# Optimization experiments

Hardware: AMD Instinct MI355X
Metric: run time of the kernel (lower is better)

Reference implementation:

```python
import jax, jax.numpy as jnp
import numpy as np
from jax import lax

NUM_CLASSES = 21
MAX_OUT = 5          # max_output_size in tf.image.non_max_suppression
IOU_THR = 0.5        # NMS_IOU_THRESHOLD
CONF_THR = 0.5       # CONFIDENCE_THRESHOLD
NEG = -1e9           # stand-in for -inf score (suppressed / background)


def setup_inputs() -> dict:
    key = jax.random.key(0)
    k1, k2, k3 = jax.random.split(key, 3)
    B, N, C = 128, 8732, NUM_CLASSES
    logits = jax.random.normal(k1, (B, N, 4 + C), dtype=jnp.float32)
    # default boxes in corner format [ymin, xmin, ymax, xmax], valid geometry
    ctr = jax.random.uniform(k2, (N, 2), dtype=jnp.float32)                 # cy, cx
    sz = jax.random.uniform(k3, (N, 2), dtype=jnp.float32, minval=0.05, maxval=0.3)  # h, w
    default_boxes = jnp.clip(
        jnp.concatenate([ctr - sz / 2, ctr + sz / 2], axis=-1), 0.0, 1.0)
    return {"logits": logits, "default_boxes": default_boxes}


def _decode(loc, db):
    # db: [N,4] corners -> center/size (matches get_offset's tf.stack)
    cy = (db[:, 2] + db[:, 0]) / 2
    cx = (db[:, 3] + db[:, 1]) / 2
    h = db[:, 2] - db[:, 0]
    w = db[:, 3] - db[:, 1]
    # loc: [B,N,4] = (dy, dx, dh, dw)
    ncy = loc[..., 0] * h + cy
    ncx = loc[..., 1] * w + cx
    nh = jnp.exp(loc[..., 2]) * h
    nw = jnp.exp(loc[..., 3]) * w
    boxes = jnp.stack(
        [ncy - nh / 2, ncx - nw / 2, ncy + nh / 2, ncx + nw / 2], axis=-1)
    return jnp.clip(boxes, 0.0, 1.0)


def _iou_one_vs_all(box, boxes):
    # box [4], boxes [N,4], corner format
    tl = jnp.maximum(box[:2], boxes[:, :2])
    br = jnp.minimum(box[2:], boxes[:, 2:])
    wh = jnp.maximum(br - tl, 0.0)
    inter = wh[:, 0] * wh[:, 1]
    a1 = (box[2] - box[0]) * (box[3] - box[1])
    a2 = (boxes[:, 2] - boxes[:, 0]) * (boxes[:, 3] - boxes[:, 1])
    return inter / (a1 + a2 - inter + 1e-12)


def _nms_single(boxes, scores, classes_f):
    # boxes [N,4], scores [N] (background already set to NEG), classes_f [N] float
    def step(s, _):
        i = jnp.argmax(s)
        sc = s[i]
        b = boxes[i]
        valid = sc > CONF_THR  # score_threshold in tf NMS
        iou = _iou_one_vs_all(b, boxes)
        s = jnp.where(iou > IOU_THR, NEG, s)  # suppresses i too (IoU=1)
        return s, (b, classes_f[i], sc, valid)

    _, (bs, cs, ss, vs) = lax.scan(step, scores, None, length=MAX_OUT)
    # pad invalid slots with zeros (TF returns variable-length; we use fixed 5 + zero pad)
    bs = jnp.where(vs[:, None], bs, 0.0)
    cs = jnp.where(vs, cs, 0.0)
    ss = jnp.where(vs, ss, 0.0)
    return bs, cs[:, None], ss[:, None]  # [5,4], [5,1], [5,1]


def reference(logits, default_boxes):
    boxes = _decode(logits[..., :4], default_boxes)          # [B,N,4]
    probs = jax.nn.softmax(logits[..., 4:], axis=-1)         # [B,N,C]
    scores = jnp.max(probs, axis=-1)                          # [B,N]
    classes = jnp.argmax(probs, axis=-1)                      # [B,N] int
    # boolean_mask(classes != 0) expressed as score = -inf for background
    scores_eff = jnp.where(classes != 0, scores, NEG)
    det_b, det_c, det_s = jax.vmap(_nms_single)(
        boxes, scores_eff, classes.astype(jnp.float32))
    # pack detection_boxes / detection_classes / detection_scores -> [B,5,6]
    return jnp.concatenate([det_b, det_c, det_s], axis=-1)
```

## Files before the change

### kernel.cpp

```cpp
#include <hip/hip_runtime.h>

#define NEG (-1e9f)
constexpr int NCLS   = 21;
constexpr int NBOX   = 8732;
constexpr int MAXOUT = 5;
constexpr int CAP    = NBOX;
constexpr float IOU_THR  = 0.5f;
constexpr float CONF_THR = 0.5f;

__global__ __launch_bounds__(256) void decode_kernel(
        const float* __restrict__ logits,
        const float4* __restrict__ dbox4,
        float4* __restrict__ cand,
        int* __restrict__ cnt,
        int BN) {
    __shared__ float sl[4][64 * 25];
    const int t    = threadIdx.x;
    const int wave = t >> 6;
    const int lane = t & 63;
    float* slw = sl[wave];

    const long long waveBox = ((long long)blockIdx.x * 4 + wave) * 64;
    if (waveBox >= BN) return;
    const long long gF     = waveBox * 25;
    const long long totalF = (long long)BN * 25;

    if (waveBox + 64 <= BN) {
        const float* gbase = logits + gF;
#pragma unroll
        for (int c = 0; c < 25; c++) {
            __builtin_amdgcn_global_load_lds(
                (const __attribute__((address_space(1))) void*)(gbase + c * 64 + lane),
                (__attribute__((address_space(3))) void*)(slw + c * 64),
                4, 0, 0);
        }
    } else {
        for (int j = lane; j < 64 * 25; j += 64) {
            long long g = gF + j;
            slw[j] = (g < totalF) ? logits[g] : 0.f;
        }
    }
    __builtin_amdgcn_s_waitcnt(0x0F70);
    __builtin_amdgcn_sched_barrier(0);

    const long long i = waveBox + lane;
    if (i >= BN) return;
    const float* L = slw + lane * 25;
    const int n = (int)(i % NBOX);
    const int b = (int)(i / NBOX);

    float4 db = dbox4[n];
    float cy = (db.z + db.x) * 0.5f;
    float cx = (db.w + db.y) * 0.5f;
    float h  = db.z - db.x;
    float w  = db.w - db.y;
    float ncy = L[0] * h + cy;
    float ncx = L[1] * w + cx;
    float nh  = expf(L[2]) * h;
    float nw  = expf(L[3]) * w;
    float y1 = fminf(fmaxf(ncy - nh * 0.5f, 0.f), 1.f);
    float x1 = fminf(fmaxf(ncx - nw * 0.5f, 0.f), 1.f);
    float y2 = fminf(fmaxf(ncy + nh * 0.5f, 0.f), 1.f);
    float x2 = fminf(fmaxf(ncx + nw * 0.5f, 0.f), 1.f);

    float m = L[4];
    int am = 0;
#pragma unroll
    for (int j = 1; j < NCLS; j++) {
        float x = L[4 + j];
        if (x > m) { m = x; am = j; }
    }
    float sum = 0.f;
#pragma unroll
    for (int j = 0; j < NCLS; j++) sum += expf(L[4 + j] - m);
    float score = 1.0f / sum;

    if (am != 0 && score > CONF_THR) {
        int p = atomicAdd(&cnt[b], 1);
        if (p < CAP) {
            float4* c = cand + ((long long)b * CAP + p) * 2;
            c[0] = make_float4(y1, x1, y2, x2);
            c[1] = make_float4(score, (float)am, (float)n, 0.f);
        }
    }
}

__global__ __launch_bounds__(64) void nms_kernel(
        const float4* __restrict__ cand,
        const int* __restrict__ cnt,
        float* __restrict__ out) {
    const int b    = blockIdx.x;
    const int lane = threadIdx.x;
    __shared__ float s_sc[CAP];
    __shared__ float s_id[CAP];

    const int M = min(cnt[b], CAP);
    const float4* cb = cand + (long long)b * CAP * 2;
    float* o = out + (long long)b * MAXOUT * 6;

    for (int i = lane; i < M; i += 64) {
        float4 mrec = cb[i * 2 + 1];
        s_sc[i] = mrec.x;
        s_id[i] = mrec.z;
    }

    int k = 0;
    for (; k < MAXOUT; k++) {
        float bv = -INFINITY, boid = 3.0e38f;
        int bi = -1;
        for (int i = lane; i < M; i += 64) {
            float v = s_sc[i], oid = s_id[i];
            if (v > bv || (v == bv && oid < boid)) { bv = v; boid = oid; bi = i; }
        }
        for (int mm = 32; mm >= 1; mm >>= 1) {
            float v2 = __shfl_xor(bv,   mm, 64);
            float o2 = __shfl_xor(boid, mm, 64);
            int   i2 = __shfl_xor(bi,   mm, 64);
            if (v2 > bv || (v2 == bv && o2 < boid)) { bv = v2; boid = o2; bi = i2; }
        }
        if (bi < 0 || !(bv > CONF_THR)) break;

        float4 sb = cb[bi * 2];
        if (lane == 0) {
            float4 mm2 = cb[bi * 2 + 1];
            o[k * 6 + 0] = sb.x; o[k * 6 + 1] = sb.y;
            o[k * 6 + 2] = sb.z; o[k * 6 + 3] = sb.w;
            o[k * 6 + 4] = mm2.y; o[k * 6 + 5] = bv;
        }

        float a1 = (sb.z - sb.x) * (sb.w - sb.y);
        for (int i = lane; i < M; i += 64) {
            float4 c = cb[i * 2];
            float tly = fmaxf(sb.x, c.x);
            float tlx = fmaxf(sb.y, c.y);
            float bry = fminf(sb.z, c.z);
            float brx = fminf(sb.w, c.w);
            float wh0 = fmaxf(bry - tly, 0.f);
            float wh1 = fmaxf(brx - tlx, 0.f);
            float inter = wh0 * wh1;
            float a2 = (c.z - c.x) * (c.w - c.y);
            float iou = inter / (a1 + a2 - inter + 1e-12f);
            if (iou > IOU_THR) s_sc[i] = NEG;
        }
    }
    for (int j = k * 6 + lane; j < MAXOUT * 6; j += 64) o[j] = 0.f;
}

extern "C" void kernel_launch(void* const* d_in, const int* in_sizes, int n_in,
                              void* d_out, int out_size, void* d_ws, size_t ws_size,
                              hipStream_t stream) {
    const float* logits = (const float*)d_in[0];
    const float4* dbox4 = (const float4*)d_in[1];
    float* out          = (float*)d_out;

    const int N  = in_sizes[1] / 4;
    const int B  = in_sizes[0] / (N * 25);
    const int BN = B * N;

    int* cnt = (int*)d_ws;
    float4* cand = (float4*)((char*)d_ws + (((size_t)B * sizeof(int) + 15) & ~(size_t)15));

    hipMemsetAsync(cnt, 0, (size_t)B * sizeof(int), stream);
    decode_kernel<<<(BN + 255) / 256, 256, 0, stream>>>(logits, dbox4, cand, cnt, BN);
    nms_kernel<<<B, 64, 0, stream>>>(cand, cnt, out);
}
```

Before: 194.8 us.

## Load four boxes per thread via float4 registers instead of LDS staging

Each thread now reads four consecutive boxes' logits (100 floats, 16-byte aligned) with 25 float4 loads straight into registers and decodes them, replacing the per-wave global-to-LDS async copy. This drops LDS usage and the wait on async loads, and uses wider vector loads. The cost is high register pressure (100 floats per thread), which may lower occupancy, and strided per-thread float4 accesses that coalesce less well across lanes.

```diff
diff --git a/kernel.cpp b/kernel.cpp
--- a/kernel.cpp
+++ b/kernel.cpp
@@ -8,71 +8,39 @@
 constexpr float IOU_THR  = 0.5f;
 constexpr float CONF_THR = 0.5f;
 
-__global__ __launch_bounds__(256) void decode_kernel(
-        const float* __restrict__ logits,
+__device__ __forceinline__ void process_box(
+        const float* __restrict__ v,
+        int idx,
         const float4* __restrict__ dbox4,
         float4* __restrict__ cand,
-        int* __restrict__ cnt,
-        int BN) {
-    __shared__ float sl[4][64 * 25];
-    const int t    = threadIdx.x;
-    const int wave = t >> 6;
-    const int lane = t & 63;
-    float* slw = sl[wave];
-
-    const long long waveBox = ((long long)blockIdx.x * 4 + wave) * 64;
-    if (waveBox >= BN) return;
-    const long long gF     = waveBox * 25;
-    const long long totalF = (long long)BN * 25;
-
-    if (waveBox + 64 <= BN) {
-        const float* gbase = logits + gF;
-#pragma unroll
-        for (int c = 0; c < 25; c++) {
-            __builtin_amdgcn_global_load_lds(
-                (const __attribute__((address_space(1))) void*)(gbase + c * 64 + lane),
-                (__attribute__((address_space(3))) void*)(slw + c * 64),
-                4, 0, 0);
-        }
-    } else {
-        for (int j = lane; j < 64 * 25; j += 64) {
-            long long g = gF + j;
-            slw[j] = (g < totalF) ? logits[g] : 0.f;
-        }
-    }
-    __builtin_amdgcn_s_waitcnt(0x0F70);
-    __builtin_amdgcn_sched_barrier(0);
-
-    const long long i = waveBox + lane;
-    if (i >= BN) return;
-    const float* L = slw + lane * 25;
-    const int n = (int)(i % NBOX);
-    const int b = (int)(i / NBOX);
+        int* __restrict__ cnt) {
+    const int n = idx % NBOX;
+    const int b = idx / NBOX;
 
     float4 db = dbox4[n];
     float cy = (db.z + db.x) * 0.5f;
     float cx = (db.w + db.y) * 0.5f;
     float h  = db.z - db.x;
     float w  = db.w - db.y;
-    float ncy = L[0] * h + cy;
-    float ncx = L[1] * w + cx;
-    float nh  = expf(L[2]) * h;
-    float nw  = expf(L[3]) * w;
+    float ncy = v[0] * h + cy;
+    float ncx = v[1] * w + cx;
+    float nh  = expf(v[2]) * h;
+    float nw  = expf(v[3]) * w;
     float y1 = fminf(fmaxf(ncy - nh * 0.5f, 0.f), 1.f);
     float x1 = fminf(fmaxf(ncx - nw * 0.5f, 0.f), 1.f);
     float y2 = fminf(fmaxf(ncy + nh * 0.5f, 0.f), 1.f);
     float x2 = fminf(fmaxf(ncx + nw * 0.5f, 0.f), 1.f);
 
-    float m = L[4];
+    float m = v[4];
     int am = 0;
 #pragma unroll
     for (int j = 1; j < NCLS; j++) {
-        float x = L[4 + j];
+        float x = v[4 + j];
         if (x > m) { m = x; am = j; }
     }
     float sum = 0.f;
 #pragma unroll
-    for (int j = 0; j < NCLS; j++) sum += expf(L[4 + j] - m);
+    for (int j = 0; j < NCLS; j++) sum += expf(v[4 + j] - m);
     float score = 1.0f / sum;
 
     if (am != 0 && score > CONF_THR) {
@@ -81,6 +49,38 @@
             float4* c = cand + ((long long)b * CAP + p) * 2;
             c[0] = make_float4(y1, x1, y2, x2);
             c[1] = make_float4(score, (float)am, (float)n, 0.f);
+        }
+    }
+}
+
+__global__ __launch_bounds__(128) void decode_kernel(
+        const float* __restrict__ logits,
+        const float4* __restrict__ dbox4,
+        float4* __restrict__ cand,
+        int* __restrict__ cnt,
+        int BN) {
+    const int g = (blockIdx.x * 128 + threadIdx.x) * 4;
+    if (g >= BN) return;
+
+    if (g + 3 < BN) {
+        const float4* f4 = (const float4*)(logits + (long long)g * 25);
+        float v[100];
+#pragma unroll
+        for (int k = 0; k < 25; k++) {
+            float4 r = f4[k];
+            v[4 * k + 0] = r.x; v[4 * k + 1] = r.y;
+            v[4 * k + 2] = r.z; v[4 * k + 3] = r.w;
+        }
+#pragma unroll
+        for (int j = 0; j < 4; j++)
+            process_box(v + 25 * j, g + j, dbox4, cand, cnt);
+    } else {
+        for (int j = 0; j < 4 && g + j < BN; j++) {
+            const float* L = logits + (long long)(g + j) * 25;
+            float v[25];
+#pragma unroll
+            for (int k = 0; k < 25; k++) v[k] = L[k];
+            process_box(v, g + j, dbox4, cand, cnt);
         }
     }
 }
@@ -161,6 +161,7 @@
     float4* cand = (float4*)((char*)d_ws + (((size_t)B * sizeof(int) + 15) & ~(size_t)15));
 
     hipMemsetAsync(cnt, 0, (size_t)B * sizeof(int), stream);
-    decode_kernel<<<(BN + 255) / 256, 256, 0, stream>>>(logits, dbox4, cand, cnt, BN);
+    const int nthreads = (BN + 3) / 4;
+    decode_kernel<<<(nthreads + 127) / 128, 128, 0, stream>>>(logits, dbox4, cand, cnt, BN);
     nms_kernel<<<B, 64, 0, stream>>>(cand, cnt, out);
 }
```

Measured after the change: 192.9 us. No clear change (-1.0%).
